# Optimization experiments

Measured on AMD Instinct MI355X. Metric: run time of the kernel, lower is better.

The kernel has to match this reference:

```python
import jax, jax.numpy as jnp
import numpy as np

DEPTH, DIM, DFF, VOCAB = 4, 512, 2048, 4096
EPS = 1e-5

def layernorm(x, w, b):
    mu = jnp.mean(x, axis=-1, keepdims=True)
    var = jnp.mean((x - mu) ** 2, axis=-1, keepdims=True)
    return (x - mu) * jax.lax.rsqrt(var + EPS) * w + b

def sconv(x, phazor_c, last_conv_c):
    # x: [B,L,dim] real; phazor_c, last_conv_c: [dim] complex
    B, L, D = x.shape
    r = jnp.abs(phazor_c)
    p = jnp.tanh(r) * jnp.exp(1j * jnp.angle(phazor_c))          # [dim]
    prog = p[None, :] ** jnp.arange(L, dtype=jnp.float32)[:, None]  # [L,dim]
    filt_fft = jnp.fft.fft(prog, n=2 * L, axis=0)                # [2L,dim]
    x_fft = jnp.fft.fft(x.astype(jnp.complex64), n=2 * L, axis=1)  # [B,2L,dim]
    conv = jnp.fft.ifft(filt_fft[None] * x_fft, axis=1)[:, :L]   # [B,L,dim]
    conv = conv + last_conv_c[None, None, :] * prog[None] * p[None, None, :]
    return conv.real.astype(x.dtype)

def setup_inputs() -> dict:
    key = jax.random.key(0)
    ks = jax.random.split(key, 20)
    f32 = jnp.float32
    inp = {}
    inp['x'] = jax.random.normal(ks[0], (2, 4096, VOCAB), dtype=f32)
    inp['Win'] = jax.random.normal(ks[1], (DIM, VOCAB), dtype=f32) * VOCAB ** -0.5
    inp['bin'] = jnp.zeros((DIM,), f32)
    inp['ln1_w'] = jnp.ones((DEPTH, DIM), f32)
    inp['ln1_b'] = jnp.zeros((DEPTH, DIM), f32)
    # phazor init: exp(2*pi*i*arange/dim)*|randn|
    ang = 2 * np.pi * jnp.arange(DIM, dtype=f32) / DIM
    mag = jnp.abs(jax.random.normal(ks[2], (DEPTH, DIM), dtype=f32))
    inp['phz_re'] = mag * jnp.cos(ang)[None]
    inp['phz_im'] = mag * jnp.sin(ang)[None]
    inp['lc_re'] = jax.random.normal(ks[3], (DEPTH, DIM), dtype=f32)
    inp['lc_im'] = jax.random.normal(ks[4], (DEPTH, DIM), dtype=f32)
    inp['sc_lin'] = jnp.ones((DEPTH, DIM), f32)
    inp['ln2_w'] = jnp.ones((DEPTH, DIM), f32)
    inp['ln2_b'] = jnp.zeros((DEPTH, DIM), f32)
    inp['W1'] = jax.random.normal(ks[5], (DEPTH, DFF, DIM), dtype=f32) * DIM ** -0.5
    inp['b1'] = jnp.zeros((DEPTH, DFF), f32)
    inp['W2'] = jax.random.normal(ks[6], (DEPTH, DIM, DFF), dtype=f32) * DFF ** -0.5
    inp['b2'] = jnp.zeros((DEPTH, DIM), f32)
    inp['lnl_w'] = jnp.ones((DIM,), f32)
    inp['lnl_b'] = jnp.zeros((DIM,), f32)
    inp['Wout'] = jax.random.normal(ks[7], (VOCAB, DIM), dtype=f32) * DIM ** -0.5
    inp['bout'] = jnp.zeros((VOCAB,), f32)
    return inp

def _forward(x, Win, bin, ln1_w, ln1_b, phz_re, phz_im, lc_re, lc_im, sc_lin,
             ln2_w, ln2_b, W1, b1, W2, b2, lnl_w, lnl_b, Wout, bout):
    h = jnp.einsum('blv,dv->bld', x, Win) + bin  # token_in

    def body(h, p):
        l1w, l1b, pr, pi, lr, li, scl, l2w, l2b, w1, b1_, w2, b2_ = p
        y = jax.nn.silu(layernorm(h, l1w, l1b))
        y = sconv(y, pr + 1j * pi, lr + 1j * li)
        h = h + y * scl
        y = layernorm(h, l2w, l2b)
        y = jax.nn.silu(jnp.einsum('bld,fd->blf', y, w1) + b1_)
        y = jnp.einsum('blf,df->bld', y, w2) + b2_
        return h + y, None

    xs = (ln1_w, ln1_b, phz_re, phz_im, lc_re, lc_im, sc_lin,
          ln2_w, ln2_b, W1, b1, W2, b2)
    h, _ = jax.lax.scan(body, h, xs)
    h = layernorm(h, lnl_w, lnl_b)
    return jnp.einsum('bld,vd->blv', h, Wout) + bout

def reference(x, Win, bin, ln1_w, ln1_b, phz_re, phz_im, lc_re, lc_im, sc_lin,
              ln2_w, ln2_b, W1, b1, W2, b2, lnl_w, lnl_b, Wout, bout):
    return _forward(x, Win, bin, ln1_w, ln1_b, phz_re, phz_im, lc_re, lc_im,
                    sc_lin, ln2_w, ln2_b, W1, b1, W2, b2, lnl_w, lnl_b, Wout, bout)
```

## Files before the change

kernel.cpp:

```cpp
#include <hip/hip_runtime.h>
#include <hip/hip_bf16.h>
#include <cstdint>
#include <cstddef>

#define DEPTH 4
#define DIM 512
#define DFF 2048
#define VOCAB 4096
#define NB 2
#define LSEQ 4096
#define MR (NB*LSEQ)
#define EPSL 1e-5f
#define NC 128
#define TCH 32

typedef __attribute__((ext_vector_type(8))) short  s8v;
typedef __attribute__((ext_vector_type(4))) float  f4v;
typedef __attribute__((ext_vector_type(8))) __bf16 bf8v;

__device__ __forceinline__ unsigned short f2b(float f) {
  union { float f; unsigned int u; } v; v.f = f;
  unsigned int r = v.u + 0x7FFFu + ((v.u >> 16) & 1u);
  return (unsigned short)(r >> 16);
}

__device__ __forceinline__ void gld16(const void* g, void* l) {
  __builtin_amdgcn_global_load_lds(
      (const __attribute__((address_space(1))) unsigned int*)(uintptr_t)g,
      (__attribute__((address_space(3))) unsigned int*)(uintptr_t)l,
      16, 0, 0);
}

template<int N> __device__ __forceinline__ void wvm() {
  if constexpr (N == 8)      asm volatile("s_waitcnt vmcnt(8)" ::: "memory");
  else if constexpr (N == 4) asm volatile("s_waitcnt vmcnt(4)" ::: "memory");
  else                       asm volatile("s_waitcnt vmcnt(0)" ::: "memory");
}

__global__ void __launch_bounds__(256) cvt_f32_bf16(
    const float* __restrict__ in, unsigned short* __restrict__ out, int n8)
{
  int i = blockIdx.x * 256 + threadIdx.x;
  if (i >= n8) return;
  const f4v* p = (const f4v*)(in + (size_t)i * 8);
  f4v a = p[0], b = p[1];
  s8v o;
  o[0]=(short)f2b(a[0]); o[1]=(short)f2b(a[1]); o[2]=(short)f2b(a[2]); o[3]=(short)f2b(a[3]);
  o[4]=(short)f2b(b[0]); o[5]=(short)f2b(b[1]); o[6]=(short)f2b(b[2]); o[7]=(short)f2b(b[3]);
  *(s8v*)(out + (size_t)i * 8) = o;
}

template<int MODE>
__global__ void __launch_bounds__(256) ln_kernel(
    const float* __restrict__ x, const float* __restrict__ w, const float* __restrict__ b,
    float* __restrict__ outf, unsigned short* __restrict__ outb)
{
  int row  = blockIdx.x * 4 + (threadIdx.x >> 6);
  int lane = threadIdx.x & 63;
  const float* xp = x + (size_t)row * DIM + lane * 8;
  f4v v0 = *(const f4v*)xp;
  f4v v1 = *(const f4v*)(xp + 4);
  float s = 0.f, s2 = 0.f;
#pragma unroll
  for (int j = 0; j < 4; ++j) { s += v0[j]; s2 += v0[j]*v0[j]; s += v1[j]; s2 += v1[j]*v1[j]; }
#pragma unroll
  for (int off = 32; off; off >>= 1) { s += __shfl_xor(s, off, 64); s2 += __shfl_xor(s2, off, 64); }
  float mu = s * (1.f / DIM);
  float rs = rsqrtf(s2 * (1.f / DIM) - mu * mu + EPSL);
  int c = lane * 8;
  f4v w0 = *(const f4v*)(w + c), w1 = *(const f4v*)(w + c + 4);
  f4v b0 = *(const f4v*)(b + c), b1 = *(const f4v*)(b + c + 4);
  float ov[8];
#pragma unroll
  for (int j = 0; j < 8; ++j) {
    float xv = (j < 4) ? v0[j] : v1[j - 4];
    float wv = (j < 4) ? w0[j] : w1[j - 4];
    float bv = (j < 4) ? b0[j] : b1[j - 4];
    float o = (xv - mu) * rs * wv + bv;
    if (MODE == 0) o = o / (1.f + __expf(-o));
    ov[j] = o;
  }
  if (MODE == 0) {
    f4v o0 = {ov[0], ov[1], ov[2], ov[3]};
    f4v o1 = {ov[4], ov[5], ov[6], ov[7]};
    *(f4v*)(outf + (size_t)row * DIM + c)     = o0;
    *(f4v*)(outf + (size_t)row * DIM + c + 4) = o1;
  } else {
    s8v o;
#pragma unroll
    for (int j = 0; j < 8; ++j) o[j] = (short)f2b(ov[j]);
    *(s8v*)(outb + (size_t)row * DIM + c) = o;
  }
}

__device__ __forceinline__ void phz2p(float re, float im, float& pre, float& pim) {
  float r = sqrtf(re * re + im * im);
  float t = (r > 1e-20f) ? (tanhf(r) / r) : 1.0f;
  pre = t * re; pim = t * im;
}

__global__ void __launch_bounds__(256) scan_a(
    const float* __restrict__ y, const float* __restrict__ pr, const float* __restrict__ pi,
    float* __restrict__ stA)
{
  int d = blockIdx.z * 256 + threadIdx.x;
  int b = blockIdx.y, c = blockIdx.x;
  float pre, pim; phz2p(pr[d], pi[d], pre, pim);
  const float* yp = y + ((size_t)b * LSEQ + (size_t)c * TCH) * DIM + d;
  float sre = 0.f, sim = 0.f;
#pragma unroll 8
  for (int j = 0; j < TCH; ++j) {
    float xv = yp[(size_t)j * DIM];
    float nre = fmaf(pre, sre, fmaf(-pim, sim, xv));
    float nim = fmaf(pre, sim, pim * sre);
    sre = nre; sim = nim;
  }
  size_t o = (((size_t)b * NC + c) * DIM + d) * 2;
  stA[o] = sre; stA[o + 1] = sim;
}

__global__ void __launch_bounds__(256) scan_b(
    const float* __restrict__ stA, float* __restrict__ carry,
    const float* __restrict__ pr, const float* __restrict__ pi,
    const float* __restrict__ lcr, const float* __restrict__ lci)
{
  int idx = blockIdx.x * 256 + threadIdx.x;
  int b = idx >> 9, d = idx & (DIM - 1);
  float pre, pim; phz2p(pr[d], pi[d], pre, pim);
  float qre = pre, qim = pim;
#pragma unroll
  for (int t = 0; t < 5; ++t) { float nr = qre*qre - qim*qim; float ni = 2.f*qre*qim; qre = nr; qim = ni; }
  float cre = lcr[d], cim = lci[d];
#pragma unroll 4
  for (int c = 0; c < NC; ++c) {
    size_t o = (((size_t)b * NC + c) * DIM + d) * 2;
    carry[o] = cre; carry[o + 1] = cim;
    float are = stA[o], aim = stA[o + 1];
    float nr = fmaf(qre, cre, fmaf(-qim, cim, are));
    float ni = fmaf(qre, cim, fmaf(qim, cre, aim));
    cre = nr; cim = ni;
  }
}

__global__ void __launch_bounds__(256) scan_c(
    const float* __restrict__ y, float* __restrict__ h, const float* __restrict__ carry,
    const float* __restrict__ pr, const float* __restrict__ pi,
    const float* __restrict__ scl)
{
  int d = blockIdx.z * 256 + threadIdx.x;
  int b = blockIdx.y, c = blockIdx.x;
  float pre, pim; phz2p(pr[d], pi[d], pre, pim);
  size_t o = (((size_t)b * NC + c) * DIM + d) * 2;
  float sre = carry[o], sim = carry[o + 1];
  float sc = scl[d];
  const float* yp = y + ((size_t)b * LSEQ + (size_t)c * TCH) * DIM + d;
  float*       hp = h + ((size_t)b * LSEQ + (size_t)c * TCH) * DIM + d;
#pragma unroll 8
  for (int j = 0; j < TCH; ++j) {
    float xv = yp[(size_t)j * DIM];
    float nre = fmaf(pre, sre, fmaf(-pim, sim, xv));
    float nim = fmaf(pre, sim, pim * sre);
    sre = nre; sim = nim;
    hp[(size_t)j * DIM] += sre * sc;
  }
}

template<int EPI>
__global__ void __launch_bounds__(256, 3) gemm_p(
    const unsigned short* __restrict__ A, const unsigned short* __restrict__ Bm,
    const float* __restrict__ bias,
    float* __restrict__ Cf, unsigned short* __restrict__ Cb,
    int N, int Keff, int lda, int ldb)
{
  __shared__ unsigned short As[3][128 * 32];
  __shared__ unsigned short Bs[3][128 * 32];
  const int tid  = threadIdx.x;
  const int lane = tid & 63, wave = tid >> 6;
  const int wm = wave >> 1, wn = wave & 1;
  const int fr = lane & 15, fq = lane >> 4;
  const int bz = blockIdx.z;

  int bx, by;
  {
    int gx = gridDim.x;
    int nwg = gx * gridDim.y;
    int b = blockIdx.y * gx + blockIdx.x;
    int lid = (b & 7) * (nwg >> 3) + (b >> 3);
    bx = lid % gx; by = lid / gx;
  }
  const int m0 = by * 128, n0 = bx * 128;
  const int koff = bz * Keff;
  const int nkt = Keff >> 5;

  f4v acc[4][4];
#pragma unroll
  for (int i = 0; i < 4; ++i)
#pragma unroll
    for (int j = 0; j < 4; ++j) acc[i][j] = (f4v){0.f, 0.f, 0.f, 0.f};

  const int row2 = tid >> 2, col2 = (tid & 3) << 3;
  auto stage = [&](int buf, int kt) {
    const unsigned short* Ab = A  + (size_t)m0 * lda + koff + kt * 32;
    const unsigned short* Bb = Bm + (size_t)n0 * ldb + koff + kt * 32;
    gld16(Ab + (size_t)row2 * lda + col2,        &As[buf][tid * 8]);
    gld16(Ab + (size_t)(row2 + 64) * lda + col2, &As[buf][(256 + tid) * 8]);
    gld16(Bb + (size_t)row2 * ldb + col2,        &Bs[buf][tid * 8]);
    gld16(Bb + (size_t)(row2 + 64) * ldb + col2, &Bs[buf][(256 + tid) * 8]);
  };

  stage(0, 0);
  stage(1, 1);

  int b0 = 0, b1 = 1, b2 = 2;
  for (int kt = 0; kt < nkt; ++kt) {
    bool pf = (kt + 2 < nkt);
    if (pf) stage(b2, kt + 2);
    if (pf)                    wvm<8>();
    else if (kt + 1 < nkt)     wvm<4>();
    else                       wvm<0>();
    __builtin_amdgcn_s_barrier();
    __builtin_amdgcn_sched_barrier(0);
    bf8v av[4], bv[4];
#pragma unroll
    for (int i = 0; i < 4; ++i)
      av[i] = *(const bf8v*)&As[b0][(wm * 64 + i * 16 + fr) * 32 + fq * 8];
#pragma unroll
    for (int j = 0; j < 4; ++j)
      bv[j] = *(const bf8v*)&Bs[b0][(wn * 64 + j * 16 + fr) * 32 + fq * 8];
#pragma unroll
    for (int i = 0; i < 4; ++i)
#pragma unroll
      for (int j = 0; j < 4; ++j)
        acc[i][j] = __builtin_amdgcn_mfma_f32_16x16x32_bf16(av[i], bv[j], acc[i][j], 0, 0, 0);
    __builtin_amdgcn_sched_barrier(0);
    __builtin_amdgcn_s_barrier();
    int t = b0; b0 = b1; b1 = b2; b2 = t;
  }

  const size_t pbase = (EPI == 3) ? (size_t)bz * MR * N : 0;
#pragma unroll
  for (int j = 0; j < 4; ++j) {
    const int col = n0 + wn * 64 + j * 16 + fr;
    const float bsv = (EPI == 3) ? 0.f : bias[col];
#pragma unroll
    for (int i = 0; i < 4; ++i) {
#pragma unroll
      for (int r = 0; r < 4; ++r) {
        const int row = m0 + wm * 64 + i * 16 + fq * 4 + r;
        const size_t off = (size_t)row * N + col;
        float v = acc[i][j][r] + bsv;
        if constexpr (EPI == 0) {
          Cf[off] = v;
        } else if constexpr (EPI == 1) {
          float sv = v / (1.f + __expf(-v));
          Cb[off] = f2b(sv);
        } else {
          Cf[pbase + off] = v;
        }
      }
    }
  }
}

template<int RES>
__global__ void __launch_bounds__(256) reduce_sk(
    const float* __restrict__ parts, const float* __restrict__ bias,
    float* __restrict__ out)
{
  size_t i = ((size_t)blockIdx.x * 256 + threadIdx.x) * 4;
  const size_t st = (size_t)MR * DIM;
  f4v v = *(const f4v*)(parts + i);
  v += *(const f4v*)(parts + st + i);
  v += *(const f4v*)(parts + 2 * st + i);
  v += *(const f4v*)(parts + 3 * st + i);
  int c = (int)(i & (DIM - 1));
  v += *(const f4v*)(bias + c);
  if (RES) v += *(const f4v*)(out + i);
  *(f4v*)(out + i) = v;
}

extern "C" void kernel_launch(void* const* d_in, const int* in_sizes, int n_in,
                              void* d_out, int out_size, void* d_ws, size_t ws_size,
                              hipStream_t stream)
{
  (void)in_sizes; (void)n_in; (void)out_size; (void)ws_size;
  const float* x    = (const float*)d_in[0];
  const float* Win  = (const float*)d_in[1];
  const float* bin  = (const float*)d_in[2];
  const float* ln1w = (const float*)d_in[3];
  const float* ln1b = (const float*)d_in[4];
  const float* phzr = (const float*)d_in[5];
  const float* phzi = (const float*)d_in[6];
  const float* lcr  = (const float*)d_in[7];
  const float* lci  = (const float*)d_in[8];
  const float* scl  = (const float*)d_in[9];
  const float* ln2w = (const float*)d_in[10];
  const float* ln2b = (const float*)d_in[11];
  const float* W1   = (const float*)d_in[12];
  const float* b1   = (const float*)d_in[13];
  const float* W2   = (const float*)d_in[14];
  const float* b2   = (const float*)d_in[15];
  const float* lnlw = (const float*)d_in[16];
  const float* lnlb = (const float*)d_in[17];
  const float* Wout = (const float*)d_in[18];
  const float* bout = (const float*)d_in[19];

  char* wsp = (char*)d_ws;
  auto alloc = [&](size_t bytes) { char* p = wsp; wsp += (bytes + 255) & ~(size_t)255; return p; };
  float*          h     = (float*)alloc((size_t)MR * DIM * 4);
  float*          y     = (float*)alloc((size_t)MR * DIM * 4);
  unsigned short* yb    = (unsigned short*)alloc((size_t)MR * DIM * 2);
  unsigned short* Winb  = (unsigned short*)alloc((size_t)DIM * VOCAB * 2);
  unsigned short* W1b   = (unsigned short*)alloc((size_t)DEPTH * DFF * DIM * 2);
  unsigned short* W2b   = (unsigned short*)alloc((size_t)DEPTH * DIM * DFF * 2);
  unsigned short* Woutb = (unsigned short*)alloc((size_t)VOCAB * DIM * 2);
  float*          stA   = (float*)alloc((size_t)NB * NC * DIM * 2 * 4);
  float*          carry = (float*)alloc((size_t)NB * NC * DIM * 2 * 4);

  unsigned short* xb    = (unsigned short*)d_out;
  unsigned short* act1  = (unsigned short*)d_out;
  float*          parts = (float*)((char*)d_out + ((size_t)64 << 20));

  dim3 blk(256);
  cvt_f32_bf16<<<dim3(((size_t)MR * VOCAB) / 2048), blk, 0, stream>>>(x, xb, (int)(((size_t)MR * VOCAB) / 8));
  cvt_f32_bf16<<<dim3((DIM * VOCAB) / 2048), blk, 0, stream>>>(Win, Winb, DIM * VOCAB / 8);
  cvt_f32_bf16<<<dim3((DEPTH * DFF * DIM) / 2048), blk, 0, stream>>>(W1, W1b, DEPTH * DFF * DIM / 8);
  cvt_f32_bf16<<<dim3((DEPTH * DFF * DIM) / 2048), blk, 0, stream>>>(W2, W2b, DEPTH * DIM * DFF / 8);
  cvt_f32_bf16<<<dim3((VOCAB * DIM) / 2048), blk, 0, stream>>>(Wout, Woutb, VOCAB * DIM / 8);

  gemm_p<3><<<dim3(DIM / 128, MR / 128, 4), blk, 0, stream>>>(
      xb, Winb, nullptr, parts, nullptr, DIM, VOCAB / 4, VOCAB, VOCAB);
  reduce_sk<0><<<dim3(MR * DIM / 1024), blk, 0, stream>>>(parts, bin, h);

  for (int l = 0; l < DEPTH; ++l) {
    ln_kernel<0><<<dim3(MR / 4), blk, 0, stream>>>(h, ln1w + l * DIM, ln1b + l * DIM, y, nullptr);
    scan_a<<<dim3(NC, NB, DIM / 256), blk, 0, stream>>>(y, phzr + l * DIM, phzi + l * DIM, stA);
    scan_b<<<dim3((NB * DIM) / 256), blk, 0, stream>>>(stA, carry, phzr + l * DIM, phzi + l * DIM,
                                                       lcr + l * DIM, lci + l * DIM);
    scan_c<<<dim3(NC, NB, DIM / 256), blk, 0, stream>>>(y, h, carry, phzr + l * DIM, phzi + l * DIM,
                                                        scl + l * DIM);
    ln_kernel<1><<<dim3(MR / 4), blk, 0, stream>>>(h, ln2w + l * DIM, ln2b + l * DIM, nullptr, yb);
    gemm_p<1><<<dim3(DFF / 128, MR / 128, 1), blk, 0, stream>>>(
        yb, W1b + (size_t)l * DFF * DIM, b1 + l * DFF, nullptr, act1, DFF, DIM, DIM, DIM);
    gemm_p<3><<<dim3(DIM / 128, MR / 128, 4), blk, 0, stream>>>(
        act1, W2b + (size_t)l * DIM * DFF, nullptr, parts, nullptr, DIM, DFF / 4, DFF, DFF);
    reduce_sk<1><<<dim3(MR * DIM / 1024), blk, 0, stream>>>(parts, b2 + l * DIM, h);
  }
  ln_kernel<1><<<dim3(MR / 4), blk, 0, stream>>>(h, lnlw, lnlb, nullptr, yb);
  gemm_p<0><<<dim3(VOCAB / 128, MR / 128, 1), blk, 0, stream>>>(
      yb, Woutb, bout, (float*)d_out, nullptr, VOCAB, DIM, DIM, DIM);
}
```

Baseline: 646.8 us.

## Fuse split-K reduction, layernorm, and scan stages into chunked block kernels

Merges the split-K partial reduction, residual add, LN1+SiLU and the first scan pass into one kernel per 16-row chunk, with the chunk staged in shared memory. It also fuses the scan correction pass with LN2 and the bf16 store, and the final reduction with the last layernorm. The chunk size is halved (NC 256, TCH 16) so a 512-thread block can hold a chunk in LDS, and the carry power changes to p^16 to match. This removes several full passes over the h and y activations and several kernel launches. The cost is a longer serial carry loop in scan_b and more LDS per block.

```diff
diff --git a/kernel.cpp b/kernel.cpp
--- a/kernel.cpp
+++ b/kernel.cpp
@@ -11,8 +11,8 @@
 #define LSEQ 4096
 #define MR (NB*LSEQ)
 #define EPSL 1e-5f
-#define NC 128
-#define TCH 32
+#define NC 256
+#define TCH 16
 
 typedef __attribute__((ext_vector_type(8))) short  s8v;
 typedef __attribute__((ext_vector_type(4))) float  f4v;
@@ -35,6 +35,11 @@
   if constexpr (N == 8)      asm volatile("s_waitcnt vmcnt(8)" ::: "memory");
   else if constexpr (N == 4) asm volatile("s_waitcnt vmcnt(4)" ::: "memory");
   else                       asm volatile("s_waitcnt vmcnt(0)" ::: "memory");
+}
+
+__device__ __forceinline__ void wred64(float& s, float& s2) {
+#pragma unroll
+  for (int off = 32; off; off >>= 1) { s += __shfl_xor(s, off, 64); s2 += __shfl_xor(s2, off, 64); }
 }
 
 __global__ void __launch_bounds__(256) cvt_f32_bf16(
@@ -50,67 +55,69 @@
   *(s8v*)(out + (size_t)i * 8) = o;
 }
 
-template<int MODE>
-__global__ void __launch_bounds__(256) ln_kernel(
-    const float* __restrict__ x, const float* __restrict__ w, const float* __restrict__ b,
-    float* __restrict__ outf, unsigned short* __restrict__ outb)
-{
-  int row  = blockIdx.x * 4 + (threadIdx.x >> 6);
-  int lane = threadIdx.x & 63;
-  const float* xp = x + (size_t)row * DIM + lane * 8;
-  f4v v0 = *(const f4v*)xp;
-  f4v v1 = *(const f4v*)(xp + 4);
-  float s = 0.f, s2 = 0.f;
-#pragma unroll
-  for (int j = 0; j < 4; ++j) { s += v0[j]; s2 += v0[j]*v0[j]; s += v1[j]; s2 += v1[j]*v1[j]; }
-#pragma unroll
-  for (int off = 32; off; off >>= 1) { s += __shfl_xor(s, off, 64); s2 += __shfl_xor(s2, off, 64); }
-  float mu = s * (1.f / DIM);
-  float rs = rsqrtf(s2 * (1.f / DIM) - mu * mu + EPSL);
-  int c = lane * 8;
-  f4v w0 = *(const f4v*)(w + c), w1 = *(const f4v*)(w + c + 4);
-  f4v b0 = *(const f4v*)(b + c), b1 = *(const f4v*)(b + c + 4);
-  float ov[8];
-#pragma unroll
-  for (int j = 0; j < 8; ++j) {
-    float xv = (j < 4) ? v0[j] : v1[j - 4];
-    float wv = (j < 4) ? w0[j] : w1[j - 4];
-    float bv = (j < 4) ? b0[j] : b1[j - 4];
-    float o = (xv - mu) * rs * wv + bv;
-    if (MODE == 0) o = o / (1.f + __expf(-o));
-    ov[j] = o;
-  }
-  if (MODE == 0) {
-    f4v o0 = {ov[0], ov[1], ov[2], ov[3]};
-    f4v o1 = {ov[4], ov[5], ov[6], ov[7]};
-    *(f4v*)(outf + (size_t)row * DIM + c)     = o0;
-    *(f4v*)(outf + (size_t)row * DIM + c + 4) = o1;
-  } else {
-    s8v o;
-#pragma unroll
-    for (int j = 0; j < 8; ++j) o[j] = (short)f2b(ov[j]);
-    *(s8v*)(outb + (size_t)row * DIM + c) = o;
-  }
-}
-
 __device__ __forceinline__ void phz2p(float re, float im, float& pre, float& pim) {
   float r = sqrtf(re * re + im * im);
   float t = (r > 1e-20f) ? (tanhf(r) / r) : 1.0f;
   pre = t * re; pim = t * im;
 }
 
-__global__ void __launch_bounds__(256) scan_a(
-    const float* __restrict__ y, const float* __restrict__ pr, const float* __restrict__ pi,
-    float* __restrict__ stA)
-{
-  int d = blockIdx.z * 256 + threadIdx.x;
-  int b = blockIdx.y, c = blockIdx.x;
+template<int RES>
+__global__ void __launch_bounds__(512) red_ln_scan(
+    const float* __restrict__ parts, float* __restrict__ h, const float* __restrict__ bias,
+    const float* __restrict__ lnw, const float* __restrict__ lnb,
+    const float* __restrict__ pr, const float* __restrict__ pi,
+    float* __restrict__ y, float* __restrict__ stA)
+{
+  __shared__ float ls[TCH][DIM];
+  const int d = threadIdx.x;
+  const int c = blockIdx.x, b = blockIdx.y;
+  const size_t rbase = ((size_t)b * LSEQ + (size_t)c * TCH) * DIM + d;
+  const size_t st = (size_t)MR * DIM;
+  const float bv = bias[d];
+#pragma unroll 4
+  for (int j = 0; j < TCH; ++j) {
+    size_t o = rbase + (size_t)j * DIM;
+    float v = parts[o] + parts[st + o] + parts[2 * st + o] + parts[3 * st + o] + bv;
+    if (RES) v += h[o];
+    h[o] = v;
+    ls[j][d] = v;
+  }
+  __syncthreads();
+  const int wave = threadIdx.x >> 6, lane = threadIdx.x & 63;
+  const int c8 = lane * 8;
+  f4v w0 = *(const f4v*)(lnw + c8), w1 = *(const f4v*)(lnw + c8 + 4);
+  f4v b0 = *(const f4v*)(lnb + c8), b1 = *(const f4v*)(lnb + c8 + 4);
+#pragma unroll
+  for (int jj = 0; jj < 2; ++jj) {
+    int j = wave * 2 + jj;
+    f4v v0 = *(const f4v*)&ls[j][c8];
+    f4v v1 = *(const f4v*)&ls[j][c8 + 4];
+    float s = 0.f, s2 = 0.f;
+#pragma unroll
+    for (int q = 0; q < 4; ++q) { s += v0[q]; s2 += v0[q]*v0[q]; s += v1[q]; s2 += v1[q]*v1[q]; }
+    wred64(s, s2);
+    float mu = s * (1.f / DIM);
+    float rs = rsqrtf(s2 * (1.f / DIM) - mu * mu + EPSL);
+    f4v o0, o1;
+#pragma unroll
+    for (int q = 0; q < 4; ++q) {
+      float a = (v0[q] - mu) * rs * w0[q] + b0[q];
+      o0[q] = a / (1.f + __expf(-a));
+      float e = (v1[q] - mu) * rs * w1[q] + b1[q];
+      o1[q] = e / (1.f + __expf(-e));
+    }
+    *(f4v*)&ls[j][c8]     = o0;
+    *(f4v*)&ls[j][c8 + 4] = o1;
+    size_t yo = ((size_t)b * LSEQ + (size_t)c * TCH + j) * DIM + c8;
+    *(f4v*)(y + yo)     = o0;
+    *(f4v*)(y + yo + 4) = o1;
+  }
+  __syncthreads();
   float pre, pim; phz2p(pr[d], pi[d], pre, pim);
-  const float* yp = y + ((size_t)b * LSEQ + (size_t)c * TCH) * DIM + d;
   float sre = 0.f, sim = 0.f;
-#pragma unroll 8
+#pragma unroll
   for (int j = 0; j < TCH; ++j) {
-    float xv = yp[(size_t)j * DIM];
+    float xv = ls[j][d];
     float nre = fmaf(pre, sre, fmaf(-pim, sim, xv));
     float nim = fmaf(pre, sim, pim * sre);
     sre = nre; sim = nim;
@@ -129,7 +136,7 @@
   float pre, pim; phz2p(pr[d], pi[d], pre, pim);
   float qre = pre, qim = pim;
 #pragma unroll
-  for (int t = 0; t < 5; ++t) { float nr = qre*qre - qim*qim; float ni = 2.f*qre*qim; qre = nr; qim = ni; }
+  for (int t = 0; t < 4; ++t) { float nr = qre*qre - qim*qim; float ni = 2.f*qre*qim; qre = nr; qim = ni; }
   float cre = lcr[d], cim = lci[d];
 #pragma unroll 4
   for (int c = 0; c < NC; ++c) {
@@ -142,26 +149,98 @@
   }
 }
 
-__global__ void __launch_bounds__(256) scan_c(
+__global__ void __launch_bounds__(512) scan_c_ln2(
     const float* __restrict__ y, float* __restrict__ h, const float* __restrict__ carry,
     const float* __restrict__ pr, const float* __restrict__ pi,
-    const float* __restrict__ scl)
-{
-  int d = blockIdx.z * 256 + threadIdx.x;
-  int b = blockIdx.y, c = blockIdx.x;
+    const float* __restrict__ scl,
+    const float* __restrict__ lnw, const float* __restrict__ lnb,
+    unsigned short* __restrict__ yb)
+{
+  __shared__ float ls[TCH][DIM];
+  const int d = threadIdx.x;
+  const int c = blockIdx.x, b = blockIdx.y;
   float pre, pim; phz2p(pr[d], pi[d], pre, pim);
-  size_t o = (((size_t)b * NC + c) * DIM + d) * 2;
-  float sre = carry[o], sim = carry[o + 1];
-  float sc = scl[d];
-  const float* yp = y + ((size_t)b * LSEQ + (size_t)c * TCH) * DIM + d;
-  float*       hp = h + ((size_t)b * LSEQ + (size_t)c * TCH) * DIM + d;
-#pragma unroll 8
+  size_t co = (((size_t)b * NC + c) * DIM + d) * 2;
+  float sre = carry[co], sim = carry[co + 1];
+  const float sc = scl[d];
+  const size_t rbase = ((size_t)b * LSEQ + (size_t)c * TCH) * DIM + d;
+#pragma unroll 4
   for (int j = 0; j < TCH; ++j) {
-    float xv = yp[(size_t)j * DIM];
+    size_t o = rbase + (size_t)j * DIM;
+    float xv = y[o];
     float nre = fmaf(pre, sre, fmaf(-pim, sim, xv));
     float nim = fmaf(pre, sim, pim * sre);
     sre = nre; sim = nim;
-    hp[(size_t)j * DIM] += sre * sc;
+    float hv = h[o] + sre * sc;
+    h[o] = hv;
+    ls[j][d] = hv;
+  }
+  __syncthreads();
+  const int wave = threadIdx.x >> 6, lane = threadIdx.x & 63;
+  const int c8 = lane * 8;
+  f4v w0 = *(const f4v*)(lnw + c8), w1 = *(const f4v*)(lnw + c8 + 4);
+  f4v b0 = *(const f4v*)(lnb + c8), b1 = *(const f4v*)(lnb + c8 + 4);
+#pragma unroll
+  for (int jj = 0; jj < 2; ++jj) {
+    int j = wave * 2 + jj;
+    f4v v0 = *(const f4v*)&ls[j][c8];
+    f4v v1 = *(const f4v*)&ls[j][c8 + 4];
+    float s = 0.f, s2 = 0.f;
+#pragma unroll
+    for (int q = 0; q < 4; ++q) { s += v0[q]; s2 += v0[q]*v0[q]; s += v1[q]; s2 += v1[q]*v1[q]; }
+    wred64(s, s2);
+    float mu = s * (1.f / DIM);
+    float rs = rsqrtf(s2 * (1.f / DIM) - mu * mu + EPSL);
+    s8v o;
+#pragma unroll
+    for (int q = 0; q < 4; ++q) {
+      o[q]     = (short)f2b((v0[q] - mu) * rs * w0[q] + b0[q]);
+      o[4 + q] = (short)f2b((v1[q] - mu) * rs * w1[q] + b1[q]);
+    }
+    *(s8v*)(yb + ((size_t)b * LSEQ + (size_t)c * TCH + j) * DIM + c8) = o;
+  }
+}
+
+__global__ void __launch_bounds__(512) red_ln_final(
+    const float* __restrict__ parts, const float* __restrict__ h, const float* __restrict__ bias,
+    const float* __restrict__ lnw, const float* __restrict__ lnb,
+    unsigned short* __restrict__ yb)
+{
+  __shared__ float ls[TCH][DIM];
+  const int d = threadIdx.x;
+  const int c = blockIdx.x, b = blockIdx.y;
+  const size_t rbase = ((size_t)b * LSEQ + (size_t)c * TCH) * DIM + d;
+  const size_t st = (size_t)MR * DIM;
+  const float bv = bias[d];
+#pragma unroll 4
+  for (int j = 0; j < TCH; ++j) {
+    size_t o = rbase + (size_t)j * DIM;
+    float v = parts[o] + parts[st + o] + parts[2 * st + o] + parts[3 * st + o] + bv + h[o];
+    ls[j][d] = v;
+  }
+  __syncthreads();
+  const int wave = threadIdx.x >> 6, lane = threadIdx.x & 63;
+  const int c8 = lane * 8;
+  f4v w0 = *(const f4v*)(lnw + c8), w1 = *(const f4v*)(lnw + c8 + 4);
+  f4v b0 = *(const f4v*)(lnb + c8), b1 = *(const f4v*)(lnb + c8 + 4);
+#pragma unroll
+  for (int jj = 0; jj < 2; ++jj) {
+    int j = wave * 2 + jj;
+    f4v v0 = *(const f4v*)&ls[j][c8];
+    f4v v1 = *(const f4v*)&ls[j][c8 + 4];
+    float s = 0.f, s2 = 0.f;
+#pragma unroll
+    for (int q = 0; q < 4; ++q) { s += v0[q]; s2 += v0[q]*v0[q]; s += v1[q]; s2 += v1[q]*v1[q]; }
+    wred64(s, s2);
+    float mu = s * (1.f / DIM);
+    float rs = rsqrtf(s2 * (1.f / DIM) - mu * mu + EPSL);
+    s8v o;
+#pragma unroll
+    for (int q = 0; q < 4; ++q) {
+      o[q]     = (short)f2b((v0[q] - mu) * rs * w0[q] + b0[q]);
+      o[4 + q] = (short)f2b((v1[q] - mu) * rs * w1[q] + b1[q]);
+    }
+    *(s8v*)(yb + ((size_t)b * LSEQ + (size_t)c * TCH + j) * DIM + c8) = o;
   }
 }
 
@@ -260,23 +339,6 @@
       }
     }
   }
-}
-
-template<int RES>
-__global__ void __launch_bounds__(256) reduce_sk(
-    const float* __restrict__ parts, const float* __restrict__ bias,
-    float* __restrict__ out)
-{
-  size_t i = ((size_t)blockIdx.x * 256 + threadIdx.x) * 4;
-  const size_t st = (size_t)MR * DIM;
-  f4v v = *(const f4v*)(parts + i);
-  v += *(const f4v*)(parts + st + i);
-  v += *(const f4v*)(parts + 2 * st + i);
-  v += *(const f4v*)(parts + 3 * st + i);
-  int c = (int)(i & (DIM - 1));
-  v += *(const f4v*)(bias + c);
-  if (RES) v += *(const f4v*)(out + i);
-  *(f4v*)(out + i) = v;
 }
 
 extern "C" void kernel_launch(void* const* d_in, const int* in_sizes, int n_in,
@@ -322,6 +384,8 @@
   float*          parts = (float*)((char*)d_out + ((size_t)64 << 20));
 
   dim3 blk(256);
+  dim3 fblk(512);
+  dim3 fgrid(NC, NB);
   cvt_f32_bf16<<<dim3(((size_t)MR * VOCAB) / 2048), blk, 0, stream>>>(x, xb, (int)(((size_t)MR * VOCAB) / 8));
   cvt_f32_bf16<<<dim3((DIM * VOCAB) / 2048), blk, 0, stream>>>(Win, Winb, DIM * VOCAB / 8);
   cvt_f32_bf16<<<dim3((DEPTH * DFF * DIM) / 2048), blk, 0, stream>>>(W1, W1b, DEPTH * DFF * DIM / 8);
@@ -330,23 +394,24 @@
 
   gemm_p<3><<<dim3(DIM / 128, MR / 128, 4), blk, 0, stream>>>(
       xb, Winb, nullptr, parts, nullptr, DIM, VOCAB / 4, VOCAB, VOCAB);
-  reduce_sk<0><<<dim3(MR * DIM / 1024), blk, 0, stream>>>(parts, bin, h);
+  red_ln_scan<0><<<fgrid, fblk, 0, stream>>>(parts, h, bin, ln1w, ln1b, phzr, phzi, y, stA);
 
   for (int l = 0; l < DEPTH; ++l) {
-    ln_kernel<0><<<dim3(MR / 4), blk, 0, stream>>>(h, ln1w + l * DIM, ln1b + l * DIM, y, nullptr);
-    scan_a<<<dim3(NC, NB, DIM / 256), blk, 0, stream>>>(y, phzr + l * DIM, phzi + l * DIM, stA);
     scan_b<<<dim3((NB * DIM) / 256), blk, 0, stream>>>(stA, carry, phzr + l * DIM, phzi + l * DIM,
                                                        lcr + l * DIM, lci + l * DIM);
-    scan_c<<<dim3(NC, NB, DIM / 256), blk, 0, stream>>>(y, h, carry, phzr + l * DIM, phzi + l * DIM,
-                                                        scl + l * DIM);
-    ln_kernel<1><<<dim3(MR / 4), blk, 0, stream>>>(h, ln2w + l * DIM, ln2b + l * DIM, nullptr, yb);
+    scan_c_ln2<<<fgrid, fblk, 0, stream>>>(y, h, carry, phzr + l * DIM, phzi + l * DIM,
+                                           scl + l * DIM, ln2w + l * DIM, ln2b + l * DIM, yb);
     gemm_p<1><<<dim3(DFF / 128, MR / 128, 1), blk, 0, stream>>>(
         yb, W1b + (size_t)l * DFF * DIM, b1 + l * DFF, nullptr, act1, DFF, DIM, DIM, DIM);
     gemm_p<3><<<dim3(DIM / 128, MR / 128, 4), blk, 0, stream>>>(
         act1, W2b + (size_t)l * DIM * DFF, nullptr, parts, nullptr, DIM, DFF / 4, DFF, DFF);
-    reduce_sk<1><<<dim3(MR * DIM / 1024), blk, 0, stream>>>(parts, b2 + l * DIM, h);
-  }
-  ln_kernel<1><<<dim3(MR / 4), blk, 0, stream>>>(h, lnlw, lnlb, nullptr, yb);
+    if (l < DEPTH - 1) {
+      red_ln_scan<1><<<fgrid, fblk, 0, stream>>>(parts, h, b2 + l * DIM,
+                                                 ln1w + (l + 1) * DIM, ln1b + (l + 1) * DIM,
+                                                 phzr + (l + 1) * DIM, phzi + (l + 1) * DIM, y, stA);
+    }
+  }
+  red_ln_final<<<fgrid, fblk, 0, stream>>>(parts, h, b2 + (DEPTH - 1) * DIM, lnlw, lnlb, yb);
   gemm_p<0><<<dim3(VOCAB / 128, MR / 128, 1), blk, 0, stream>>>(
       yb, Woutb, bout, (float*)d_out, nullptr, VOCAB, DIM, DIM, DIM);
 }
```

Result: slower. 661.1 us (+2.2%).
